# Optimization experiments

Hardware: AMD Instinct MI355X
Metric: run time of the kernel (lower is better)

The kernel has to match this reference:

```python
import jax, jax.numpy as jnp
import numpy as np

B, NINP, NHID = 8192, 256, 1024
NB_IN, NB_OUT = 1, 8
BS_OUT = NHID // NB_OUT          # 128
ATT_OUT = BS_OUT * 4             # 512
TOPKVAL = 4


@jax.custom_vjp
def blocked_grad(x, mask):
    # forward is identity; backward masks the gradient (RIMs blocked_grad)
    return x

def _bg_fwd(x, mask):
    return x, mask

def _bg_bwd(mask, g):
    return (g * mask, jnp.zeros_like(mask))

blocked_grad.defvjp(_bg_fwd, _bg_bwd)


def setup_inputs() -> dict:
    key = jax.random.key(0)
    ks = jax.random.split(key, 12)
    p = lambda i, shape, s: s * jax.random.normal(ks[i], shape, dtype=jnp.float32)
    return {
        "inp": jax.random.normal(ks[0], (B, NB_IN * NINP), dtype=jnp.float32),
        "hx": jax.random.normal(ks[1], (B, NHID), dtype=jnp.float32),
        "step": 0,
        "Wq1": p(2, (NB_OUT, BS_OUT, 64), 0.01),
        "Wk1": p(3, (2, NINP, 64), 0.01),
        "Wv1": p(4, (2, NINP, ATT_OUT), 0.01),
        "Wq2": p(5, (NB_OUT, BS_OUT, 64), 0.01),
        "Wk2": p(6, (NB_OUT, BS_OUT, 64), 0.01),
        "Wv2": p(7, (NB_OUT, BS_OUT, 64), 0.01),
        "fc_w": p(8, (64, BS_OUT), 0.05),
        "fc_b": jnp.zeros((BS_OUT,), jnp.float32),
        "gate_w": p(9, (64, BS_OUT), 0.05),
        "gate_b": jnp.zeros((BS_OUT,), jnp.float32),
        "gru_wi": p(10, (NB_OUT, ATT_OUT, 3 * BS_OUT), 0.05),
        "gru_wh": p(11, (NB_OUT, BS_OUT, 3 * BS_OUT), 0.05),
        "gru_bi": jnp.zeros((NB_OUT, 3 * BS_OUT), jnp.float32),
        "gru_bh": jnp.zeros((NB_OUT, 3 * BS_OUT), jnp.float32),
    }


def _block_gru(x, h, wi, wh, bi, bh):
    # x: [B, K, ATT_OUT], h: [B, K, BS_OUT]; blockified GRUCell == per-block GRU
    gx = jnp.einsum('bkd,kde->bke', x, wi) + bi
    gh = jnp.einsum('bkd,kde->bke', h, wh) + bh
    xr, xz, xn = jnp.split(gx, 3, axis=-1)
    hr, hz, hn = jnp.split(gh, 3, axis=-1)
    r = jax.nn.sigmoid(xr + hr)
    z = jax.nn.sigmoid(xz + hz)
    n = jnp.tanh(xn + r * hn)
    return (1.0 - z) * n + z * h


def reference(inp, hx, step, Wq1, Wk1, Wv1, Wq2, Wk2, Wv2,
              fc_w, fc_b, gate_w, gate_b, gru_wi, gru_wh, gru_bi, gru_bh):
    b = inp.shape[0]
    x = inp.reshape(b, NB_IN, NINP)                              # repeat factor (num_modules_read_input-1)=1
    kv = jnp.concatenate([jnp.zeros_like(x[:, :1]), x], axis=1)  # [b, 2, NINP] (null slot first)
    hq = hx.reshape(b, NB_OUT, BS_OUT)

    # input attention (n_head=1, d_k=64, skip_write -> identity fc, no residual gating)
    q = jnp.einsum('bkd,kde->bke', hq, Wq1)                      # [b, 8, 64]
    kk = jnp.einsum('bmd,mde->bme', kv, Wk1)                     # [b, 2, 64]
    vv = jnp.einsum('bmd,mde->bme', kv, Wv1)                     # [b, 2, 512]
    iatt = jax.nn.softmax(jnp.einsum('bke,bme->bkm', q, kk) / 8.0, axis=-1)  # temp=sqrt(64)
    inp_use = jnp.einsum('bkm,bme->bke', iatt, vv)               # [b, 8, 512]

    # top-k block selection: zero out blocks most attentive to the null slot
    null_score = iatt[:, :, 0]
    _, bottom_idx = jax.lax.top_k(null_score, NB_OUT - TOPKVAL)
    mask = jnp.ones((b, NB_OUT), inp.dtype)
    mask = mask.at[jnp.arange(b)[:, None], bottom_idx].set(0.0)
    mask = jax.lax.stop_gradient(mask)

    hx_new = _block_gru(inp_use, hq, gru_wi, gru_wh, gru_bi, gru_bh)  # [b, 8, 128]

    # communication attention (n_head=4, d_k=d_v=16, gated residual form)
    g = blocked_grad(hx_new, mask[:, :, None])
    q2 = jnp.einsum('bkd,kde->bke', g, Wq2).reshape(b, NB_OUT, 4, 16)
    k2 = jnp.einsum('bkd,kde->bke', g, Wk2).reshape(b, NB_OUT, 4, 16)
    v2 = jnp.einsum('bkd,kde->bke', g, Wv2).reshape(b, NB_OUT, 4, 16)
    attn2 = jax.nn.softmax(jnp.einsum('bqhd,bkhd->bhqk', q2, k2) / 4.0, axis=-1)  # temp=sqrt(16)
    o = jnp.einsum('bhqk,bkhd->bqhd', attn2, v2).reshape(b, NB_OUT, 64)
    att = jax.nn.sigmoid(o @ gate_w + gate_b) * jnp.tanh(o @ fc_w + fc_b)  # [b, 8, 128]
    hx_new = hx_new + att

    mask_full = jnp.repeat(mask[:, :, None], BS_OUT, axis=2).reshape(b, NHID)
    hx_out = mask_full * hx_new.reshape(b, NHID) + (1.0 - mask_full) * hx
    return hx_out, mask_full
```

## Files before the change

kernel.cpp:

```cpp
#include <hip/hip_runtime.h>
#include <cstdint>
#include <cstddef>

#define NB 8192

typedef __attribute__((ext_vector_type(4))) float f32x4;
typedef __attribute__((ext_vector_type(8))) short bf16x8;

__device__ __forceinline__ float sigmoidf_(float x){ return 1.0f/(1.0f+expf(-x)); }

__device__ __forceinline__ unsigned short f2bf(float f){
    union { float f; unsigned u; } v; v.f = f;
    unsigned u = v.u;
    return (unsigned short)((u + 0x7fffu + ((u >> 16) & 1u)) >> 16);
}
__device__ __forceinline__ float bf2f(unsigned short b){
    union { unsigned u; float f; } v; v.u = ((unsigned)b) << 16;
    return v.f;
}
__device__ __forceinline__ void ld8f(const unsigned short* p, float* f){
    uint4 u = *(const uint4*)p;
    f[0]=bf2f(u.x&0xffff); f[1]=bf2f(u.x>>16);
    f[2]=bf2f(u.y&0xffff); f[3]=bf2f(u.y>>16);
    f[4]=bf2f(u.z&0xffff); f[5]=bf2f(u.z>>16);
    f[6]=bf2f(u.w&0xffff); f[7]=bf2f(u.w>>16);
}

__global__ __launch_bounds__(256) void gemm_nn_d(
    const float* __restrict__ A, int lda, int aZ,
    const float* __restrict__ W, int wZ, int ldw,
    float* __restrict__ C, int ldc, int cZ,
    int K)
{
    __shared__ float As[16][68];
    __shared__ float Ws[16][64];
    const int tid = threadIdx.x;
    const int tx = tid & 15, ty = tid >> 4;
    const int rowBase = blockIdx.y * 64;
    const int colBase = blockIdx.x * 64;
    A += (size_t)blockIdx.z * aZ;
    W += (size_t)blockIdx.z * wZ;
    C += (size_t)blockIdx.z * cZ;

    double acc[4][4] = {};
    for (int k0 = 0; k0 < K; k0 += 16) {
#pragma unroll
        for (int i = 0; i < 4; ++i) {
            int e = i * 256 + tid;
            int m = e >> 4, kk = e & 15;
            As[kk][m] = A[(size_t)(rowBase + m) * lda + (k0 + kk)];
        }
#pragma unroll
        for (int i = 0; i < 4; ++i) {
            int e = i * 256 + tid;
            int kk = e >> 6, n = e & 63;
            Ws[kk][n] = W[(size_t)(k0 + kk) * ldw + (colBase + n)];
        }
        __syncthreads();
#pragma unroll
        for (int kk = 0; kk < 16; ++kk) {
            const float4 a4 = *(const float4*)&As[kk][ty * 4];
            const float4 b4 = *(const float4*)&Ws[kk][tx * 4];
            const float a[4] = {a4.x, a4.y, a4.z, a4.w};
            const float b[4] = {b4.x, b4.y, b4.z, b4.w};
#pragma unroll
            for (int i = 0; i < 4; ++i)
#pragma unroll
                for (int j = 0; j < 4; ++j)
                    acc[i][j] = fma((double)a[i], (double)b[j], acc[i][j]);
        }
        __syncthreads();
    }
#pragma unroll
    for (int i = 0; i < 4; ++i) {
        float* Cr = C + (size_t)(rowBase + ty * 4 + i) * ldc + colBase + tx * 4;
#pragma unroll
        for (int j = 0; j < 4; ++j) Cr[j] = (float)acc[i][j];
    }
}

__global__ __launch_bounds__(256) void score_mask_k(
    const float* __restrict__ qbuf,
    const float* __restrict__ kk1,
    float* __restrict__ cbuf,
    float* __restrict__ maskb)
{
    const int b = blockIdx.x * 256 + threadIdx.x;
    const float* kr = kk1 + (size_t)b * 64;
    double s[8];
#pragma unroll
    for (int k = 0; k < 8; ++k) {
        const float* qr = qbuf + (size_t)b * 512 + k * 64;
        double acc = 0.0;
#pragma unroll
        for (int d = 0; d < 64; ++d) acc = fma((double)qr[d], (double)kr[d], acc);
        s[k] = acc / 8.0;
    }
#pragma unroll
    for (int k = 0; k < 8; ++k) {
        int rank = 0;
#pragma unroll
        for (int j = 0; j < 8; ++j)
            rank += (s[j] < s[k]) || (s[j] == s[k] && j < k);
        maskb[(size_t)b * 8 + k] = (rank < 4) ? 0.f : 1.f;
        cbuf[(size_t)b * 8 + k] = (float)(1.0 / (1.0 + exp(-s[k])));
    }
}

__global__ __launch_bounds__(256) void prep_w(
    const float* __restrict__ gwi, const float* __restrict__ gwh,
    const float* __restrict__ Wq2, const float* __restrict__ Wk2, const float* __restrict__ Wv2,
    const float* __restrict__ gate_w, const float* __restrict__ fc_w,
    unsigned short* __restrict__ wi_t,
    unsigned short* __restrict__ wh_t,
    unsigned short* __restrict__ w2_t,
    unsigned short* __restrict__ gfc_t)
{
    int idx = blockIdx.x * 256 + threadIdx.x;
    const int N1 = 8*384*512, N2 = 8*384*128, N3 = 8*192*128, N4 = 2*128*64;
    if (idx < N1) {
        int k = idx / 196608, r = idx % 196608, j = r / 512, e = r % 512;
        wi_t[idx] = f2bf(gwi[((size_t)k*512 + e)*384 + j]); return;
    }
    idx -= N1;
    if (idx < N2) {
        int k = idx / 49152, r = idx % 49152, j = r / 128, d = r % 128;
        wh_t[idx] = f2bf(gwh[((size_t)k*128 + d)*384 + j]); return;
    }
    idx -= N2;
    if (idx < N3) {
        int k = idx / 24576, r = idx % 24576, n = r / 128, d = r % 128;
        const float* Wsrc = (n < 64) ? Wq2 : ((n < 128) ? Wk2 : Wv2);
        w2_t[idx] = f2bf(Wsrc[((size_t)k*128 + d)*64 + (n & 63)]); return;
    }
    idx -= N3;
    if (idx < N4) {
        int g = idx / 8192, r = idx % 8192, j = r / 64, d = r % 64;
        gfc_t[idx] = f2bf((g ? fc_w : gate_w)[d*128 + j]);
    }
}

template<int ASRC_F32, int EPI>
__global__ __launch_bounds__(256) void gemm_bf(
    const void* __restrict__ Av, int lda, int aZ,
    const unsigned short* __restrict__ Bt, int bZ, int ldb,
    unsigned short* __restrict__ C, int ldc, long cZ,
    int K)
{
    __shared__ unsigned short As[64][72];
    __shared__ unsigned short Bs[64][72];
    const int tid = threadIdx.x;
    const int wave = tid >> 6, lane = tid & 63;
    const int wr = wave >> 1, wc = wave & 1;
    const int lr = lane & 15, lo = lane >> 4;
    const int rowBase = blockIdx.y * 64, colBase = blockIdx.x * 64;
    const int z = blockIdx.z;

    const f32x4 zero = {0.f, 0.f, 0.f, 0.f};
    f32x4 acc[2][2];
    acc[0][0]=zero; acc[0][1]=zero; acc[1][0]=zero; acc[1][1]=zero;

    const unsigned short* B = Bt + (size_t)z * bZ;
    for (int k0 = 0; k0 < K; k0 += 64) {
        if (ASRC_F32) {
            const float* A = (const float*)Av + (size_t)z * aZ;
#pragma unroll
            for (int i = 0; i < 4; ++i) {
                int c = i*256 + tid;
                int r = c >> 4, kc = (c & 15) << 2;
                float4 a4 = *(const float4*)(A + (size_t)(rowBase + r) * lda + k0 + kc);
                unsigned short* p = &As[r][kc];
                p[0]=f2bf(a4.x); p[1]=f2bf(a4.y); p[2]=f2bf(a4.z); p[3]=f2bf(a4.w);
            }
        } else {
            const unsigned short* A = (const unsigned short*)Av + (size_t)z * aZ;
#pragma unroll
            for (int i = 0; i < 2; ++i) {
                int c = i*256 + tid;
                int r = c >> 3, kc = (c & 7) << 3;
                *(uint4*)&As[r][kc] = *(const uint4*)(A + (size_t)(rowBase + r) * lda + k0 + kc);
            }
        }
#pragma unroll
        for (int i = 0; i < 2; ++i) {
            int c = i*256 + tid;
            int n = c >> 3, kc = (c & 7) << 3;
            *(uint4*)&Bs[n][kc] = *(const uint4*)(B + (size_t)(colBase + n) * ldb + k0 + kc);
        }
        __syncthreads();
#pragma unroll
        for (int ks = 0; ks < 64; ks += 32) {
            bf16x8 a0 = *(const bf16x8*)&As[wr*32 + lr][ks + lo*8];
            bf16x8 a1 = *(const bf16x8*)&As[wr*32 + 16 + lr][ks + lo*8];
            bf16x8 b0 = *(const bf16x8*)&Bs[wc*32 + lr][ks + lo*8];
            bf16x8 b1 = *(const bf16x8*)&Bs[wc*32 + 16 + lr][ks + lo*8];
            acc[0][0] = __builtin_amdgcn_mfma_f32_16x16x32_bf16(a0,b0,acc[0][0],0,0,0);
            acc[0][1] = __builtin_amdgcn_mfma_f32_16x16x32_bf16(a0,b1,acc[0][1],0,0,0);
            acc[1][0] = __builtin_amdgcn_mfma_f32_16x16x32_bf16(a1,b0,acc[1][0],0,0,0);
            acc[1][1] = __builtin_amdgcn_mfma_f32_16x16x32_bf16(a1,b1,acc[1][1],0,0,0);
        }
        __syncthreads();
    }
#pragma unroll
    for (int i = 0; i < 2; ++i)
#pragma unroll
    for (int j = 0; j < 2; ++j)
#pragma unroll
    for (int r = 0; r < 4; ++r) {
        int row = rowBase + wr*32 + i*16 + lo*4 + r;
        int col = colBase + wc*32 + j*16 + lr;
        float v = acc[i][j][r];
        if (EPI == 0) C[(size_t)row * ldc + (size_t)z * cZ + col] = f2bf(v);
        else          C[(size_t)z * cZ + (size_t)col * ldc + row] = f2bf(v);
    }
}

__global__ __launch_bounds__(256) void gemm_gxh(
    const float* __restrict__ inp,
    const unsigned short* __restrict__ wc_t,
    const float* __restrict__ hx,
    const unsigned short* __restrict__ wh_t,
    const float* __restrict__ cbuf,
    const float* __restrict__ gbi, const float* __restrict__ gbh,
    unsigned short* __restrict__ comb)
{
    __shared__ unsigned short As[64][72];
    __shared__ unsigned short Bs[64][72];
    const int tid = threadIdx.x;
    const int wave = tid >> 6, lane = tid & 63;
    const int wr = wave >> 1, wc = wave & 1;
    const int lr = lane & 15, lo = lane >> 4;
    const int rowBase = blockIdx.y * 64, colBase = blockIdx.x * 64;
    const int z = blockIdx.z;

    const f32x4 zero = {0.f, 0.f, 0.f, 0.f};
    f32x4 acc1[2][2], acc2[2][2];
    acc1[0][0]=zero; acc1[0][1]=zero; acc1[1][0]=zero; acc1[1][1]=zero;
    acc2[0][0]=zero; acc2[0][1]=zero; acc2[1][0]=zero; acc2[1][1]=zero;

    const unsigned short* B1 = wc_t + (size_t)z * (384*256);
    for (int k0 = 0; k0 < 256; k0 += 64) {
#pragma unroll
        for (int i = 0; i < 4; ++i) {
            int c = i*256 + tid;
            int r = c >> 4, kc = (c & 15) << 2;
            float4 a4 = *(const float4*)(inp + (size_t)(rowBase + r) * 256 + k0 + kc);
            unsigned short* p = &As[r][kc];
            p[0]=f2bf(a4.x); p[1]=f2bf(a4.y); p[2]=f2bf(a4.z); p[3]=f2bf(a4.w);
        }
#pragma unroll
        for (int i = 0; i < 2; ++i) {
            int c = i*256 + tid;
            int n = c >> 3, kc = (c & 7) << 3;
            *(uint4*)&Bs[n][kc] = *(const uint4*)(B1 + (size_t)(colBase + n) * 256 + k0 + kc);
        }
        __syncthreads();
#pragma unroll
        for (int ks = 0; ks < 64; ks += 32) {
            bf16x8 a0 = *(const bf16x8*)&As[wr*32 + lr][ks + lo*8];
            bf16x8 a1 = *(const bf16x8*)&As[wr*32 + 16 + lr][ks + lo*8];
            bf16x8 b0 = *(const bf16x8*)&Bs[wc*32 + lr][ks + lo*8];
            bf16x8 b1 = *(const bf16x8*)&Bs[wc*32 + 16 + lr][ks + lo*8];
            acc1[0][0] = __builtin_amdgcn_mfma_f32_16x16x32_bf16(a0,b0,acc1[0][0],0,0,0);
            acc1[0][1] = __builtin_amdgcn_mfma_f32_16x16x32_bf16(a0,b1,acc1[0][1],0,0,0);
            acc1[1][0] = __builtin_amdgcn_mfma_f32_16x16x32_bf16(a1,b0,acc1[1][0],0,0,0);
            acc1[1][1] = __builtin_amdgcn_mfma_f32_16x16x32_bf16(a1,b1,acc1[1][1],0,0,0);
        }
        __syncthreads();
    }
    const unsigned short* B2 = wh_t + (size_t)z * (384*128);
    for (int k0 = 0; k0 < 128; k0 += 64) {
#pragma unroll
        for (int i = 0; i < 4; ++i) {
            int c = i*256 + tid;
            int r = c >> 4, kc = (c & 15) << 2;
            float4 a4 = *(const float4*)(hx + (size_t)(rowBase + r) * 1024 + z*128 + k0 + kc);
            unsigned short* p = &As[r][kc];
            p[0]=f2bf(a4.x); p[1]=f2bf(a4.y); p[2]=f2bf(a4.z); p[3]=f2bf(a4.w);
        }
#pragma unroll
        for (int i = 0; i < 2; ++i) {
            int c = i*256 + tid;
            int n = c >> 3, kc = (c & 7) << 3;
            *(uint4*)&Bs[n][kc] = *(const uint4*)(B2 + (size_t)(colBase + n) * 128 + k0 + kc);
        }
        __syncthreads();
#pragma unroll
        for (int ks = 0; ks < 64; ks += 32) {
            bf16x8 a0 = *(const bf16x8*)&As[wr*32 + lr][ks + lo*8];
            bf16x8 a1 = *(const bf16x8*)&As[wr*32 + 16 + lr][ks + lo*8];
            bf16x8 b0 = *(const bf16x8*)&Bs[wc*32 + lr][ks + lo*8];
            bf16x8 b1 = *(const bf16x8*)&Bs[wc*32 + 16 + lr][ks + lo*8];
            acc2[0][0] = __builtin_amdgcn_mfma_f32_16x16x32_bf16(a0,b0,acc2[0][0],0,0,0);
            acc2[0][1] = __builtin_amdgcn_mfma_f32_16x16x32_bf16(a0,b1,acc2[0][1],0,0,0);
            acc2[1][0] = __builtin_amdgcn_mfma_f32_16x16x32_bf16(a1,b0,acc2[1][0],0,0,0);
            acc2[1][1] = __builtin_amdgcn_mfma_f32_16x16x32_bf16(a1,b1,acc2[1][1],0,0,0);
        }
        __syncthreads();
    }
#pragma unroll
    for (int i = 0; i < 2; ++i)
#pragma unroll
    for (int j = 0; j < 2; ++j)
#pragma unroll
    for (int r = 0; r < 4; ++r) {
        int row = rowBase + wr*32 + i*16 + lo*4 + r;
        int col = colBase + wc*32 + j*16 + lr;
        float c = cbuf[(size_t)row * 8 + z];
        float v1 = fmaf(c, acc1[i][j][r], gbi[z*384 + col]);
        float v2 = acc2[i][j][r] + gbh[z*384 + col];
        size_t base = ((size_t)z * 8192 + row) * 512;
        if (col < 256) comb[base + col] = f2bf(v1 + v2);
        else { comb[base + col] = f2bf(v1); comb[base + col + 128] = f2bf(v2); }
    }
}

__global__ __launch_bounds__(256) void gru_all(
    const unsigned short* __restrict__ comb, const float* __restrict__ hx,
    unsigned short* __restrict__ hxn)
{
    const int idx = blockIdx.x * 256 + threadIdx.x;
    const int j = idx & 127, k = (idx >> 7) & 7, b = idx >> 10;
    const size_t base = ((size_t)k * 8192 + b) * 512;
    const float rz = bf2f(comb[base + j]);
    const float zz = bf2f(comb[base + 128 + j]);
    const float xn = bf2f(comb[base + 256 + j]);
    const float hn = bf2f(comb[base + 384 + j]);
    const float r = sigmoidf_(rz), z = sigmoidf_(zz);
    const float n = tanhf(fmaf(r, hn, xn));
    const float h = hx[idx];
    hxn[idx] = f2bf((1.f - z) * n + z * h);
}

__global__ __launch_bounds__(256) void attn2_bf(
    const unsigned short* __restrict__ qkv, unsigned short* __restrict__ o)
{
    const int idx = blockIdx.x * 256 + threadIdx.x;
    const int qb = idx & 7, h = (idx >> 3) & 3, b = idx >> 5;
    const unsigned short* rowb = qkv + (size_t)b * 1536;
    float qv[16];
    ld8f(rowb + qb*192 + h*16, qv); ld8f(rowb + qb*192 + h*16 + 8, qv + 8);
    float sc[8]; float mx = -1e30f;
#pragma unroll
    for (int kb = 0; kb < 8; ++kb) {
        float kv[16];
        ld8f(rowb + kb*192 + 64 + h*16, kv); ld8f(rowb + kb*192 + 64 + h*16 + 8, kv + 8);
        float a = 0.f;
#pragma unroll
        for (int d = 0; d < 16; ++d) a = fmaf(qv[d], kv[d], a);
        sc[kb] = a * 0.25f;
        mx = fmaxf(mx, sc[kb]);
    }
    float sum = 0.f;
#pragma unroll
    for (int kb = 0; kb < 8; ++kb) { sc[kb] = expf(sc[kb] - mx); sum += sc[kb]; }
    const float inv = 1.f / sum;
    float oa[16];
#pragma unroll
    for (int d = 0; d < 16; ++d) oa[d] = 0.f;
#pragma unroll
    for (int kb = 0; kb < 8; ++kb) {
        float vv[16];
        ld8f(rowb + kb*192 + 128 + h*16, vv); ld8f(rowb + kb*192 + 128 + h*16 + 8, vv + 8);
#pragma unroll
        for (int d = 0; d < 16; ++d) oa[d] = fmaf(sc[kb], vv[d], oa[d]);
    }
    unsigned short t[16];
#pragma unroll
    for (int d = 0; d < 16; ++d) t[d] = f2bf(oa[d] * inv);
    uint4 u0, u1;
    u0.x = (unsigned)t[0] | ((unsigned)t[1]<<16);  u0.y = (unsigned)t[2] | ((unsigned)t[3]<<16);
    u0.z = (unsigned)t[4] | ((unsigned)t[5]<<16);  u0.w = (unsigned)t[6] | ((unsigned)t[7]<<16);
    u1.x = (unsigned)t[8] | ((unsigned)t[9]<<16);  u1.y = (unsigned)t[10]| ((unsigned)t[11]<<16);
    u1.z = (unsigned)t[12]| ((unsigned)t[13]<<16); u1.w = (unsigned)t[14]| ((unsigned)t[15]<<16);
    unsigned short* op = o + (size_t)(b*8 + qb) * 64 + h*16;
    *(uint4*)op = u0; *(uint4*)(op + 8) = u1;
}

__global__ __launch_bounds__(256) void gatefc_final(
    const unsigned short* __restrict__ o,
    const unsigned short* __restrict__ gfc_t,
    const float* __restrict__ gate_b, const float* __restrict__ fc_b,
    const unsigned short* __restrict__ hxn,
    const float* __restrict__ hx,
    const float* __restrict__ maskb,
    float* __restrict__ out)
{
    __shared__ unsigned short As[64][72];
    __shared__ unsigned short Bg[64][72];
    __shared__ unsigned short Bf[64][72];
    const int tid = threadIdx.x;
    const int wave = tid >> 6, lane = tid & 63;
    const int wr = wave >> 1, wc = wave & 1;
    const int lr = lane & 15, lo = lane >> 4;
    const int rowBase = blockIdx.y * 64, colBase = blockIdx.x * 64;

#pragma unroll
    for (int i = 0; i < 2; ++i) {
        int c = i*256 + tid;
        int r = c >> 3, kc = (c & 7) << 3;
        *(uint4*)&As[r][kc] = *(const uint4*)(o + (size_t)(rowBase + r) * 64 + kc);
        *(uint4*)&Bg[r][kc] = *(const uint4*)(gfc_t + (size_t)(colBase + r) * 64 + kc);
        *(uint4*)&Bf[r][kc] = *(const uint4*)(gfc_t + 8192 + (size_t)(colBase + r) * 64 + kc);
    }
    __syncthreads();

    const f32x4 zero = {0.f, 0.f, 0.f, 0.f};
    f32x4 ag[2][2], af[2][2];
    ag[0][0]=zero; ag[0][1]=zero; ag[1][0]=zero; ag[1][1]=zero;
    af[0][0]=zero; af[0][1]=zero; af[1][0]=zero; af[1][1]=zero;
#pragma unroll
    for (int ks = 0; ks < 64; ks += 32) {
        bf16x8 a0 = *(const bf16x8*)&As[wr*32 + lr][ks + lo*8];
        bf16x8 a1 = *(const bf16x8*)&As[wr*32 + 16 + lr][ks + lo*8];
        bf16x8 g0 = *(const bf16x8*)&Bg[wc*32 + lr][ks + lo*8];
        bf16x8 g1 = *(const bf16x8*)&Bg[wc*32 + 16 + lr][ks + lo*8];
        bf16x8 f0 = *(const bf16x8*)&Bf[wc*32 + lr][ks + lo*8];
        bf16x8 f1 = *(const bf16x8*)&Bf[wc*32 + 16 + lr][ks + lo*8];
        ag[0][0] = __builtin_amdgcn_mfma_f32_16x16x32_bf16(a0,g0,ag[0][0],0,0,0);
        ag[0][1] = __builtin_amdgcn_mfma_f32_16x16x32_bf16(a0,g1,ag[0][1],0,0,0);
        ag[1][0] = __builtin_amdgcn_mfma_f32_16x16x32_bf16(a1,g0,ag[1][0],0,0,0);
        ag[1][1] = __builtin_amdgcn_mfma_f32_16x16x32_bf16(a1,g1,ag[1][1],0,0,0);
        af[0][0] = __builtin_amdgcn_mfma_f32_16x16x32_bf16(a0,f0,af[0][0],0,0,0);
        af[0][1] = __builtin_amdgcn_mfma_f32_16x16x32_bf16(a0,f1,af[0][1],0,0,0);
        af[1][0] = __builtin_amdgcn_mfma_f32_16x16x32_bf16(a1,f0,af[1][0],0,0,0);
        af[1][1] = __builtin_amdgcn_mfma_f32_16x16x32_bf16(a1,f1,af[1][1],0,0,0);
    }
#pragma unroll
    for (int i = 0; i < 2; ++i)
#pragma unroll
    for (int j = 0; j < 2; ++j)
#pragma unroll
    for (int r = 0; r < 4; ++r) {
        int m   = rowBase + wr*32 + i*16 + lo*4 + r;
        int col = colBase + wc*32 + j*16 + lr;
        float g = sigmoidf_(ag[i][j][r] + gate_b[col]);
        float f = tanhf(af[i][j][r] + fc_b[col]);
        float att = g * f;
        size_t oidx = (size_t)m * 128 + col;
        float msk = maskb[m];
        float hnv = bf2f(hxn[oidx]) + att;
        out[oidx] = msk * hnv + (1.f - msk) * hx[oidx];
        out[(size_t)NB * 1024 + oidx] = msk;
    }
}

extern "C" void kernel_launch(void* const* d_in, const int* in_sizes, int n_in,
                              void* d_out, int out_size, void* d_ws, size_t ws_size,
                              hipStream_t stream)
{
    (void)in_sizes; (void)n_in; (void)out_size; (void)ws_size;
    const float* inp    = (const float*)d_in[0];
    const float* hx     = (const float*)d_in[1];
    const float* Wq1    = (const float*)d_in[3];
    const float* Wk1    = (const float*)d_in[4];
    const float* Wv1    = (const float*)d_in[5];
    const float* Wq2    = (const float*)d_in[6];
    const float* Wk2    = (const float*)d_in[7];
    const float* Wv2    = (const float*)d_in[8];
    const float* fc_w   = (const float*)d_in[9];
    const float* fc_b   = (const float*)d_in[10];
    const float* gate_w = (const float*)d_in[11];
    const float* gate_b = (const float*)d_in[12];
    const float* gwi    = (const float*)d_in[13];
    const float* gwh    = (const float*)d_in[14];
    const float* gbi    = (const float*)d_in[15];
    const float* gbh    = (const float*)d_in[16];
    float* out = (float*)d_out;

    char* W = (char*)d_ws;
    float* cbuf  = (float*)(W);
    float* maskb = (float*)(W + 262144);
    float* kk1f  = (float*)(W + 524288);
    float* qbuff = (float*)(W + 524288 + 2097152);
    unsigned short* wi_t  = (unsigned short*)(W + 524288);
    unsigned short* wh_t  = (unsigned short*)(W + 524288 + 3145728);
    unsigned short* w2_t  = (unsigned short*)(W + 524288 + 3932160);
    unsigned short* gfc_t = (unsigned short*)(W + 524288 + 4325376);
    unsigned short* wc_t  = (unsigned short*)(W + 524288 + 4358144);
    unsigned short* comb  = (unsigned short*)(W + 19398656);
    unsigned short* qkv   = (unsigned short*)(W + 19398656);
    unsigned short* o_bf  = (unsigned short*)(W + 19398656 + 25165824);
    unsigned short* hxn   = (unsigned short*)(W + 86507520);

    const dim3 blk(256);

    gemm_nn_d<<<dim3(1, 128, 1), blk, 0, stream>>>(inp, 256, 0, Wk1 + 256*64, 0, 64, kk1f, 64, 0, 256);
    gemm_nn_d<<<dim3(1, 128, 8), blk, 0, stream>>>(hx, 1024, 128, Wq1, 128*64, 64, qbuff, 512, 64, 128);
    score_mask_k<<<dim3(32), blk, 0, stream>>>(qbuff, kk1f, cbuf, maskb);

    prep_w<<<dim3(8512), blk, 0, stream>>>(gwi, gwh, Wq2, Wk2, Wv2, gate_w, fc_w,
                                           wi_t, wh_t, w2_t, gfc_t);

    gemm_bf<1, 1><<<dim3(6, 4, 8), blk, 0, stream>>>(
        Wv1 + 256*512, 512, 0, wi_t, 384*512, 512, wc_t, 256, (long)384*256, 512);

    gemm_gxh<<<dim3(6, 128, 8), blk, 0, stream>>>(inp, wc_t, hx, wh_t, cbuf, gbi, gbh, comb);

    gru_all<<<dim3(32768), blk, 0, stream>>>(comb, hx, hxn);

    gemm_bf<0, 0><<<dim3(3, 128, 8), blk, 0, stream>>>(
        hxn, 1024, 128, w2_t, 192*128, 128, qkv, 1536, 192L, 128);

    attn2_bf<<<dim3(1024), blk, 0, stream>>>(qkv, o_bf);

    gatefc_final<<<dim3(2, 1024), blk, 0, stream>>>(o_bf, gfc_t, gate_b, fc_b,
                                                    hxn, hx, maskb, out);
}
```

Baseline: 402.6 us.

## Pre-cast activations to bf16, widen gxh tile, use fp32 accumulation in small GEMMs

Adds a cast kernel that converts inp and hx to bf16 once, so the gxh GEMM loads bf16 directly instead of reconverting fp32 per tile. The gxh GEMM tile is widened from 64 to 128 columns, which halves the grid and reuses each A tile across twice as many MFMAs. The small query/key GEMMs switch from double to float accumulation, avoiding slow FP64 FMAs. The cost is an extra launch plus a bf16 buffer round trip, and the float accumulation could flip near-tie top-k mask decisions relative to the double version.

```diff
diff --git a/kernel.cpp b/kernel.cpp
--- a/kernel.cpp
+++ b/kernel.cpp
@@ -26,7 +26,7 @@
     f[6]=bf2f(u.w&0xffff); f[7]=bf2f(u.w>>16);
 }
 
-__global__ __launch_bounds__(256) void gemm_nn_d(
+__global__ __launch_bounds__(256) void gemm_nn(
     const float* __restrict__ A, int lda, int aZ,
     const float* __restrict__ W, int wZ, int ldw,
     float* __restrict__ C, int ldc, int cZ,
@@ -42,7 +42,7 @@
     W += (size_t)blockIdx.z * wZ;
     C += (size_t)blockIdx.z * cZ;
 
-    double acc[4][4] = {};
+    float acc[4][4] = {};
     for (int k0 = 0; k0 < K; k0 += 16) {
 #pragma unroll
         for (int i = 0; i < 4; ++i) {
@@ -67,7 +67,7 @@
             for (int i = 0; i < 4; ++i)
 #pragma unroll
                 for (int j = 0; j < 4; ++j)
-                    acc[i][j] = fma((double)a[i], (double)b[j], acc[i][j]);
+                    acc[i][j] = fmaf(a[i], b[j], acc[i][j]);
         }
         __syncthreads();
     }
@@ -75,7 +75,7 @@
     for (int i = 0; i < 4; ++i) {
         float* Cr = C + (size_t)(rowBase + ty * 4 + i) * ldc + colBase + tx * 4;
 #pragma unroll
-        for (int j = 0; j < 4; ++j) Cr[j] = (float)acc[i][j];
+        for (int j = 0; j < 4; ++j) Cr[j] = acc[i][j];
     }
 }
 
@@ -105,6 +105,22 @@
         maskb[(size_t)b * 8 + k] = (rank < 4) ? 0.f : 1.f;
         cbuf[(size_t)b * 8 + k] = (float)(1.0 / (1.0 + exp(-s[k])));
     }
+}
+
+__global__ __launch_bounds__(256) void cast_bf(
+    const float* __restrict__ inp, const float* __restrict__ hx,
+    unsigned short* __restrict__ inp_bf, unsigned short* __restrict__ hx_bf)
+{
+    const int idx = blockIdx.x * 256 + threadIdx.x;
+    const int NI = 524288;
+    const float* src; unsigned short* dst; int i;
+    if (idx < NI) { src = inp; dst = inp_bf; i = idx; }
+    else          { src = hx;  dst = hx_bf;  i = idx - NI; }
+    float4 v = *(const float4*)(src + (size_t)i * 4);
+    uint2 u;
+    u.x = (unsigned)f2bf(v.x) | ((unsigned)f2bf(v.y) << 16);
+    u.y = (unsigned)f2bf(v.z) | ((unsigned)f2bf(v.w) << 16);
+    *(uint2*)(dst + (size_t)i * 4) = u;
 }
 
 __global__ __launch_bounds__(256) void prep_w(
@@ -216,40 +232,42 @@
 }
 
 __global__ __launch_bounds__(256) void gemm_gxh(
-    const float* __restrict__ inp,
+    const unsigned short* __restrict__ inp_bf,
     const unsigned short* __restrict__ wc_t,
-    const float* __restrict__ hx,
+    const unsigned short* __restrict__ hx_bf,
     const unsigned short* __restrict__ wh_t,
     const float* __restrict__ cbuf,
     const float* __restrict__ gbi, const float* __restrict__ gbh,
     unsigned short* __restrict__ comb)
 {
     __shared__ unsigned short As[64][72];
-    __shared__ unsigned short Bs[64][72];
+    __shared__ unsigned short Bs[128][72];
     const int tid = threadIdx.x;
     const int wave = tid >> 6, lane = tid & 63;
     const int wr = wave >> 1, wc = wave & 1;
     const int lr = lane & 15, lo = lane >> 4;
-    const int rowBase = blockIdx.y * 64, colBase = blockIdx.x * 64;
+    const int rowBase = blockIdx.y * 64, colBase = blockIdx.x * 128;
     const int z = blockIdx.z;
 
     const f32x4 zero = {0.f, 0.f, 0.f, 0.f};
-    f32x4 acc1[2][2], acc2[2][2];
-    acc1[0][0]=zero; acc1[0][1]=zero; acc1[1][0]=zero; acc1[1][1]=zero;
-    acc2[0][0]=zero; acc2[0][1]=zero; acc2[1][0]=zero; acc2[1][1]=zero;
+    f32x4 acc1[2][2][2], acc2[2][2][2];
+#pragma unroll
+    for (int t = 0; t < 2; ++t)
+#pragma unroll
+    for (int i = 0; i < 2; ++i)
+#pragma unroll
+    for (int j = 0; j < 2; ++j) { acc1[t][i][j] = zero; acc2[t][i][j] = zero; }
 
     const unsigned short* B1 = wc_t + (size_t)z * (384*256);
     for (int k0 = 0; k0 < 256; k0 += 64) {
 #pragma unroll
+        for (int i = 0; i < 2; ++i) {
+            int c = i*256 + tid;
+            int r = c >> 3, kc = (c & 7) << 3;
+            *(uint4*)&As[r][kc] = *(const uint4*)(inp_bf + (size_t)(rowBase + r) * 256 + k0 + kc);
+        }
+#pragma unroll
         for (int i = 0; i < 4; ++i) {
-            int c = i*256 + tid;
-            int r = c >> 4, kc = (c & 15) << 2;
-            float4 a4 = *(const float4*)(inp + (size_t)(rowBase + r) * 256 + k0 + kc);
-            unsigned short* p = &As[r][kc];
-            p[0]=f2bf(a4.x); p[1]=f2bf(a4.y); p[2]=f2bf(a4.z); p[3]=f2bf(a4.w);
-        }
-#pragma unroll
-        for (int i = 0; i < 2; ++i) {
             int c = i*256 + tid;
             int n = c >> 3, kc = (c & 7) << 3;
             *(uint4*)&Bs[n][kc] = *(const uint4*)(B1 + (size_t)(colBase + n) * 256 + k0 + kc);
@@ -259,27 +277,28 @@
         for (int ks = 0; ks < 64; ks += 32) {
             bf16x8 a0 = *(const bf16x8*)&As[wr*32 + lr][ks + lo*8];
             bf16x8 a1 = *(const bf16x8*)&As[wr*32 + 16 + lr][ks + lo*8];
-            bf16x8 b0 = *(const bf16x8*)&Bs[wc*32 + lr][ks + lo*8];
-            bf16x8 b1 = *(const bf16x8*)&Bs[wc*32 + 16 + lr][ks + lo*8];
-            acc1[0][0] = __builtin_amdgcn_mfma_f32_16x16x32_bf16(a0,b0,acc1[0][0],0,0,0);
-            acc1[0][1] = __builtin_amdgcn_mfma_f32_16x16x32_bf16(a0,b1,acc1[0][1],0,0,0);
-            acc1[1][0] = __builtin_amdgcn_mfma_f32_16x16x32_bf16(a1,b0,acc1[1][0],0,0,0);
-            acc1[1][1] = __builtin_amdgcn_mfma_f32_16x16x32_bf16(a1,b1,acc1[1][1],0,0,0);
+#pragma unroll
+            for (int t = 0; t < 2; ++t) {
+                bf16x8 b0 = *(const bf16x8*)&Bs[t*64 + wc*32 + lr][ks + lo*8];
+                bf16x8 b1 = *(const bf16x8*)&Bs[t*64 + wc*32 + 16 + lr][ks + lo*8];
+                acc1[t][0][0] = __builtin_amdgcn_mfma_f32_16x16x32_bf16(a0,b0,acc1[t][0][0],0,0,0);
+                acc1[t][0][1] = __builtin_amdgcn_mfma_f32_16x16x32_bf16(a0,b1,acc1[t][0][1],0,0,0);
+                acc1[t][1][0] = __builtin_amdgcn_mfma_f32_16x16x32_bf16(a1,b0,acc1[t][1][0],0,0,0);
+                acc1[t][1][1] = __builtin_amdgcn_mfma_f32_16x16x32_bf16(a1,b1,acc1[t][1][1],0,0,0);
+            }
         }
         __syncthreads();
     }
     const unsigned short* B2 = wh_t + (size_t)z * (384*128);
     for (int k0 = 0; k0 < 128; k0 += 64) {
 #pragma unroll
+        for (int i = 0; i < 2; ++i) {
+            int c = i*256 + tid;
+            int r = c >> 3, kc = (c & 7) << 3;
+            *(uint4*)&As[r][kc] = *(const uint4*)(hx_bf + (size_t)(rowBase + r) * 1024 + z*128 + k0 + kc);
+        }
+#pragma unroll
         for (int i = 0; i < 4; ++i) {
-            int c = i*256 + tid;
-            int r = c >> 4, kc = (c & 15) << 2;
-            float4 a4 = *(const float4*)(hx + (size_t)(rowBase + r) * 1024 + z*128 + k0 + kc);
-            unsigned short* p = &As[r][kc];
-            p[0]=f2bf(a4.x); p[1]=f2bf(a4.y); p[2]=f2bf(a4.z); p[3]=f2bf(a4.w);
-        }
-#pragma unroll
-        for (int i = 0; i < 2; ++i) {
             int c = i*256 + tid;
             int n = c >> 3, kc = (c & 7) << 3;
             *(uint4*)&Bs[n][kc] = *(const uint4*)(B2 + (size_t)(colBase + n) * 128 + k0 + kc);
@@ -289,15 +308,20 @@
         for (int ks = 0; ks < 64; ks += 32) {
             bf16x8 a0 = *(const bf16x8*)&As[wr*32 + lr][ks + lo*8];
             bf16x8 a1 = *(const bf16x8*)&As[wr*32 + 16 + lr][ks + lo*8];
-            bf16x8 b0 = *(const bf16x8*)&Bs[wc*32 + lr][ks + lo*8];
-            bf16x8 b1 = *(const bf16x8*)&Bs[wc*32 + 16 + lr][ks + lo*8];
-            acc2[0][0] = __builtin_amdgcn_mfma_f32_16x16x32_bf16(a0,b0,acc2[0][0],0,0,0);
-            acc2[0][1] = __builtin_amdgcn_mfma_f32_16x16x32_bf16(a0,b1,acc2[0][1],0,0,0);
-            acc2[1][0] = __builtin_amdgcn_mfma_f32_16x16x32_bf16(a1,b0,acc2[1][0],0,0,0);
-            acc2[1][1] = __builtin_amdgcn_mfma_f32_16x16x32_bf16(a1,b1,acc2[1][1],0,0,0);
-        }
-        __syncthreads();
-    }
+#pragma unroll
+            for (int t = 0; t < 2; ++t) {
+                bf16x8 b0 = *(const bf16x8*)&Bs[t*64 + wc*32 + lr][ks + lo*8];
+                bf16x8 b1 = *(const bf16x8*)&Bs[t*64 + wc*32 + 16 + lr][ks + lo*8];
+                acc2[t][0][0] = __builtin_amdgcn_mfma_f32_16x16x32_bf16(a0,b0,acc2[t][0][0],0,0,0);
+                acc2[t][0][1] = __builtin_amdgcn_mfma_f32_16x16x32_bf16(a0,b1,acc2[t][0][1],0,0,0);
+                acc2[t][1][0] = __builtin_amdgcn_mfma_f32_16x16x32_bf16(a1,b0,acc2[t][1][0],0,0,0);
+                acc2[t][1][1] = __builtin_amdgcn_mfma_f32_16x16x32_bf16(a1,b1,acc2[t][1][1],0,0,0);
+            }
+        }
+        __syncthreads();
+    }
+#pragma unroll
+    for (int t = 0; t < 2; ++t)
 #pragma unroll
     for (int i = 0; i < 2; ++i)
 #pragma unroll
@@ -305,10 +329,10 @@
 #pragma unroll
     for (int r = 0; r < 4; ++r) {
         int row = rowBase + wr*32 + i*16 + lo*4 + r;
-        int col = colBase + wc*32 + j*16 + lr;
+        int col = colBase + t*64 + wc*32 + j*16 + lr;
         float c = cbuf[(size_t)row * 8 + z];
-        float v1 = fmaf(c, acc1[i][j][r], gbi[z*384 + col]);
-        float v2 = acc2[i][j][r] + gbh[z*384 + col];
+        float v1 = fmaf(c, acc1[t][i][j][r], gbi[z*384 + col]);
+        float v2 = acc2[t][i][j][r] + gbh[z*384 + col];
         size_t base = ((size_t)z * 8192 + row) * 512;
         if (col < 256) comb[base + col] = f2bf(v1 + v2);
         else { comb[base + col] = f2bf(v1); comb[base + col + 128] = f2bf(v2); }
@@ -469,33 +493,36 @@
     float* out = (float*)d_out;
 
     char* W = (char*)d_ws;
-    float* cbuf  = (float*)(W);
-    float* maskb = (float*)(W + 262144);
-    float* kk1f  = (float*)(W + 524288);
-    float* qbuff = (float*)(W + 524288 + 2097152);
-    unsigned short* wi_t  = (unsigned short*)(W + 524288);
-    unsigned short* wh_t  = (unsigned short*)(W + 524288 + 3145728);
-    unsigned short* w2_t  = (unsigned short*)(W + 524288 + 3932160);
-    unsigned short* gfc_t = (unsigned short*)(W + 524288 + 4325376);
-    unsigned short* wc_t  = (unsigned short*)(W + 524288 + 4358144);
-    unsigned short* comb  = (unsigned short*)(W + 19398656);
-    unsigned short* qkv   = (unsigned short*)(W + 19398656);
-    unsigned short* o_bf  = (unsigned short*)(W + 19398656 + 25165824);
-    unsigned short* hxn   = (unsigned short*)(W + 86507520);
+    float* cbuf  = (float*)(W + 0x0);
+    float* maskb = (float*)(W + 0x40000);
+    float* kk1f  = (float*)(W + 0x80000);
+    float* qbuff = (float*)(W + 0x280000);
+    unsigned short* inp_bf = (unsigned short*)(W + 0x1280000);
+    unsigned short* hx_bf  = (unsigned short*)(W + 0x1680000);
+    unsigned short* wi_t   = (unsigned short*)(W + 0x2680000);
+    unsigned short* wh_t   = (unsigned short*)(W + 0x2980000);
+    unsigned short* w2_t   = (unsigned short*)(W + 0x2A40000);
+    unsigned short* gfc_t  = (unsigned short*)(W + 0x2AA0000);
+    unsigned short* wc_t   = (unsigned short*)(W + 0x2AA8000);
+    unsigned short* comb   = (unsigned short*)(W + 0x2C28000);
+    unsigned short* hxn    = (unsigned short*)(W + 0x6C28000);
+    unsigned short* qkv    = comb;
+    unsigned short* o_bf   = (unsigned short*)(W + 0x2C28000 + 25165824);
 
     const dim3 blk(256);
 
-    gemm_nn_d<<<dim3(1, 128, 1), blk, 0, stream>>>(inp, 256, 0, Wk1 + 256*64, 0, 64, kk1f, 64, 0, 256);
-    gemm_nn_d<<<dim3(1, 128, 8), blk, 0, stream>>>(hx, 1024, 128, Wq1, 128*64, 64, qbuff, 512, 64, 128);
+    gemm_nn<<<dim3(1, 128, 1), blk, 0, stream>>>(inp, 256, 0, Wk1 + 256*64, 0, 64, kk1f, 64, 0, 256);
+    gemm_nn<<<dim3(1, 128, 8), blk, 0, stream>>>(hx, 1024, 128, Wq1, 128*64, 64, qbuff, 512, 64, 128);
     score_mask_k<<<dim3(32), blk, 0, stream>>>(qbuff, kk1f, cbuf, maskb);
 
+    cast_bf<<<dim3(10240), blk, 0, stream>>>(inp, hx, inp_bf, hx_bf);
     prep_w<<<dim3(8512), blk, 0, stream>>>(gwi, gwh, Wq2, Wk2, Wv2, gate_w, fc_w,
                                            wi_t, wh_t, w2_t, gfc_t);
 
     gemm_bf<1, 1><<<dim3(6, 4, 8), blk, 0, stream>>>(
         Wv1 + 256*512, 512, 0, wi_t, 384*512, 512, wc_t, 256, (long)384*256, 512);
 
-    gemm_gxh<<<dim3(6, 128, 8), blk, 0, stream>>>(inp, wc_t, hx, wh_t, cbuf, gbi, gbh, comb);
+    gemm_gxh<<<dim3(3, 128, 8), blk, 0, stream>>>(inp_bf, wc_t, hx_bf, wh_t, cbuf, gbi, gbh, comb);
 
     gru_all<<<dim3(32768), blk, 0, stream>>>(comb, hx, hxn);
 
```

Result: faster. 372.8 us (-7.4%).
